# Performance work log

Measured on AMD Instinct MI355X. Metric: run time of the kernel, lower is better.

Reference implementation:

```python
import jax, jax.numpy as jnp
import numpy as np

# config: nsql-350M-like, 8 layers
L, D, H, HD, FF, V, RD, MP = 8, 1024, 16, 64, 4096, 51200, 32, 4


def setup_inputs() -> dict:
    key = jax.random.key(0)
    ks = jax.random.split(key, 8)
    B, S = 1, 1024
    s = 0.02
    return {
        'idx': jax.random.randint(ks[0], (B, S), 0, V),
        'input_pos': jnp.arange(S),
        'emb': jax.random.normal(ks[1], (V, D)) * s,
        'Wqkv': jax.random.normal(ks[2], (L, 3 * D, D)) * s,
        'Wo': jax.random.normal(ks[3], (L, D, D)) * s,
        'ln1_w': jnp.ones((L, D)), 'ln1_b': jnp.zeros((L, D)),
        'fc_in_w': jax.random.normal(ks[4], (L, FF, D)) * s,
        'fc_in_b': jnp.zeros((L, FF)),
        'fc_out_w': jax.random.normal(ks[5], (L, D, FF)) * s,
        'fc_out_b': jnp.zeros((L, D)),
        'lnf_w': jnp.ones((D,)), 'lnf_b': jnp.zeros((D,)),
        'lm_w': jax.random.normal(ks[6], (V, D)) * s,
        'lm_b': jnp.zeros((V,)),
    }


def _layer_norm(x, w, b, eps=1e-5):
    mu = jnp.mean(x, axis=-1, keepdims=True)
    var = jnp.var(x, axis=-1, keepdims=True)
    return (x - mu) * jax.lax.rsqrt(var + eps) * w + b


def _new_gelu(x):
    # transformers NewGELUActivation == tanh-approx gelu
    return jax.nn.gelu(x, approximate=True)


def _sincos(input_pos):
    # create_sinusoidal_positions over rotary_dim, gathered at input_pos
    inv_freq = 1.0 / (10000.0 ** (jnp.arange(0, RD, 2, dtype=jnp.float32) / RD))
    ang = input_pos.astype(jnp.float32)[:, None] * inv_freq          # [S, RD/2]
    # repeat_interleave(..., 2, dim=-1) -> interleaved sin/cos, shape [1,S,1,RD]
    sin = jnp.repeat(jnp.sin(ang), 2, axis=-1)[None, :, None, :]
    cos = jnp.repeat(jnp.cos(ang), 2, axis=-1)[None, :, None, :]
    return sin, cos


def _rotary(x, sin, cos):
    # x: [B,S,H,HD]; GPT-J interleaved rotary on first RD dims
    xr, xp = x[..., :RD], x[..., RD:]
    x1, x2 = xr[..., ::2], xr[..., 1::2]
    rot = jnp.stack((-x2, x1), axis=-1).reshape(xr.shape)  # rotate_every_two
    return jnp.concatenate([xr * cos + rot * sin, xp], axis=-1)


def reference(idx, input_pos, emb, Wqkv, Wo, ln1_w, ln1_b, fc_in_w, fc_in_b,
              fc_out_w, fc_out_b, lnf_w, lnf_b, lm_w, lm_b):
    B, S = idx.shape
    x = emb[idx]                                        # [B,S,D]
    sin, cos = _sincos(input_pos)
    causal = jnp.tril(jnp.ones((S, S), dtype=bool))
    neg = jnp.finfo(x.dtype).min
    ld = D // MP

    def split_heads(t):
        # CodeGen _split_heads with mp_num=4: [B,S,MP,ld] -> [B,S,H,HD]
        return t.reshape(B, S, MP, H // MP, HD).reshape(B, S, H, HD)

    for l in range(L):
        h = _layer_norm(x, ln1_w[l], ln1_b[l])
        qkv = (h @ Wqkv[l].T).reshape(B, S, MP, 3 * ld)
        q, v, k = qkv[..., :ld], qkv[..., ld:2 * ld], qkv[..., 2 * ld:]  # q,v,k order!
        q = _rotary(split_heads(q), sin, cos)
        k = _rotary(split_heads(k), sin, cos)
        vh = split_heads(v)
        q, k, vh = (jnp.transpose(t, (0, 2, 1, 3)) for t in (q, k, vh))  # [B,H,S,HD]
        scores = jnp.einsum('bhqd,bhkd->bhqk', q, k) / jnp.sqrt(jnp.asarray(HD, x.dtype))
        scores = jnp.where(causal, scores, neg)
        att = jax.nn.softmax(scores, axis=-1)
        y = jnp.einsum('bhqk,bhkd->bhqd', att, vh)
        y = jnp.transpose(y, (0, 2, 1, 3)).reshape(B, S, D)
        attn_out = y @ Wo[l].T
        mlp = _new_gelu(h @ fc_in_w[l].T + fc_in_b[l]) @ fc_out_w[l].T + fc_out_b[l]
        x = attn_out + mlp + x                          # parallel block + residual

    x = _layer_norm(x, lnf_w, lnf_b)
    return x @ lm_w.T + lm_b                            # [B,S,V]
```

## Files before the change

### kernel.cpp

```cpp
#include <hip/hip_runtime.h>

#define SQ 1024
#define DIM 1024
#define NH 16
#define HDIM 64
#define FFD 4096
#define NV 51200
#define NL 8
#define LDBUF 5120
#define WELEMS ((long)(3 * DIM + DIM + FFD + FFD) * DIM)

typedef __bf16 bf16x8 __attribute__((ext_vector_type(8)));
typedef float f32x4 __attribute__((ext_vector_type(4)));

__device__ __forceinline__ unsigned short f2bf(float f) {
    union { float f; unsigned int i; } v; v.f = f;
    unsigned int r = v.i + 0x7fffu + ((v.i >> 16) & 1u);
    return (unsigned short)(r >> 16);
}
__device__ __forceinline__ float gelu_tanh(float x) {
    float x3 = x * x * x;
    return 0.5f * x * (1.0f + tanhf(0.79788456080286535588f * (x + 0.044715f * x3)));
}
__device__ __forceinline__ void cvt8(const float* __restrict__ s, unsigned short* __restrict__ d, long i) {
    float4 a = *reinterpret_cast<const float4*>(s + i);
    float4 b = *reinterpret_cast<const float4*>(s + i + 4);
    bf16x8 w;
    w[0] = (__bf16)a.x; w[1] = (__bf16)a.y; w[2] = (__bf16)a.z; w[3] = (__bf16)a.w;
    w[4] = (__bf16)b.x; w[5] = (__bf16)b.y; w[6] = (__bf16)b.z; w[7] = (__bf16)b.w;
    *reinterpret_cast<bf16x8*>(d + i) = w;
}

#define GLD16(gp, lp) __builtin_amdgcn_global_load_lds( \
    (__attribute__((address_space(1))) void*)(gp), \
    (__attribute__((address_space(3))) void*)(lp), 16, 0, 0)
#define VMCNT0 asm volatile("s_waitcnt vmcnt(0)" ::: "memory")

__global__ void cvt4_kernel(const float* __restrict__ w0, const float* __restrict__ w1,
                            const float* __restrict__ w2, const float* __restrict__ w3,
                            unsigned short* __restrict__ dst) {
    const int b = blockIdx.x;
    const float* s; long off; unsigned short* d;
    if (b < 1536)      { s = w0; d = dst;                      off = (long)b * 2048; }
    else if (b < 2048) { s = w1; d = dst + (long)3072 * 1024;  off = (long)(b - 1536) * 2048; }
    else if (b < 4096) { s = w2; d = dst + (long)4096 * 1024;  off = (long)(b - 2048) * 2048; }
    else               { s = w3; d = dst + (long)8192 * 1024;  off = (long)(b - 4096) * 2048; }
    cvt8(s, d, off + threadIdx.x * 8);
}
__global__ void cvt_kernel(const float* __restrict__ src, unsigned short* __restrict__ dst) {
    cvt8(src, dst, ((long)blockIdx.x * 256 + threadIdx.x) * 8);
}

__global__ void sincos_kernel(const int* __restrict__ pos, float2* __restrict__ sc) {
    const int t = blockIdx.x * 256 + threadIdx.x;
    if (t >= SQ * 16) return;
    const int s = t >> 4, i = t & 15;
    const float ang = (float)pos[s] * powf(10000.0f, -(float)i / 16.0f);
    sc[t] = make_float2(sinf(ang), cosf(ang));
}

__global__ void embed_kernel(const int* __restrict__ idx, const float* __restrict__ emb,
                             float* __restrict__ x) {
    const int s = blockIdx.x;
    const int d = threadIdx.x * 4;
    const int row = idx[s];
    *reinterpret_cast<float4*>(x + (long)s * DIM + d) =
        *reinterpret_cast<const float4*>(emb + (long)row * DIM + d);
}

template <bool RED>
__global__ __launch_bounds__(256) void ln_kernel(float* __restrict__ x,
                                                 const float* __restrict__ part,
                                                 const float* __restrict__ w,
                                                 const float* __restrict__ b,
                                                 unsigned short* __restrict__ out) {
    __shared__ float red[8];
    const int s = blockIdx.x, tid = threadIdx.x;
    const long fidx = (long)s * 256 + tid;
    float4 v = reinterpret_cast<const float4*>(x)[fidx];
    if (RED) {
        #pragma unroll
        for (int z = 0; z < 4; z++) {
            float4 p = reinterpret_cast<const float4*>(part + (long)z * SQ * DIM)[fidx];
            v.x += p.x; v.y += p.y; v.z += p.z; v.w += p.w;
        }
        reinterpret_cast<float4*>(x)[fidx] = v;
    }
    float sum = v.x + v.y + v.z + v.w;
    float sq = v.x * v.x + v.y * v.y + v.z * v.z + v.w * v.w;
    #pragma unroll
    for (int off = 32; off; off >>= 1) { sum += __shfl_xor(sum, off); sq += __shfl_xor(sq, off); }
    const int wid = tid >> 6, lane = tid & 63;
    if (lane == 0) { red[wid * 2] = sum; red[wid * 2 + 1] = sq; }
    __syncthreads();
    sum = red[0] + red[2] + red[4] + red[6];
    sq  = red[1] + red[3] + red[5] + red[7];
    const float mu = sum * (1.0f / DIM);
    const float var = sq * (1.0f / DIM) - mu * mu;
    const float rstd = rsqrtf(var + 1e-5f);
    const int d = tid * 4;
    float vv[4] = {v.x, v.y, v.z, v.w};
    ushort4 o;
    unsigned short* op = (unsigned short*)&o;
    #pragma unroll
    for (int j = 0; j < 4; j++)
        op[j] = f2bf((vv[j] - mu) * rstd * w[d + j] + b[d + j]);
    *reinterpret_cast<ushort4*>(out + (long)s * DIM + d) = o;
}

__global__ __launch_bounds__(256) void gemm_qkv_fcin(const unsigned short* __restrict__ A,
                                                     const unsigned short* __restrict__ B1,
                                                     const unsigned short* __restrict__ B2,
                                                     const float* __restrict__ bias,
                                                     unsigned short* __restrict__ ffout,
                                                     const float2* __restrict__ sc,
                                                     unsigned short* __restrict__ qt,
                                                     unsigned short* __restrict__ kt,
                                                     unsigned short* __restrict__ vt,
                                                     const float* __restrict__ lmsrc,
                                                     unsigned short* __restrict__ lmdst) {
    __shared__ __align__(16) unsigned short As[2][128 * 64];
    __shared__ __align__(16) unsigned short Bs[2][128 * 64];
    const int tid = threadIdx.x;
    if (blockIdx.x >= 448) {
        if (lmdst) {
            const int cb = (int)blockIdx.x - 448;
            const long stride = (long)((int)gridDim.x - 448) * 256;
            const long nlmv = (long)(NV / NL) * DIM / 8;
            for (long i = (long)cb * 256 + tid; i < nlmv; i += stride) cvt8(lmsrc, lmdst, i * 8);
        }
        return;
    }
    const int sb = (blockIdx.x & 7) * 56 + (blockIdx.x >> 3);
    const int mb = sb & 7, nb = sb >> 3;
    const int m0 = mb * 128, n0 = nb * 128;
    const int lane = tid & 63, wid = tid >> 6;
    const int l15 = lane & 15, lhi = lane >> 4;
    const int wr = wid >> 1, wc = wid & 1;
    const int sw = l15 & 7;

    const unsigned short* Bbase = B1;
    int nloc = n0;
    if (nb >= 24) { Bbase = B2; nloc = n0 - 3072; }

    f32x4 acc[4][4];
    #pragma unroll
    for (int i = 0; i < 4; i++)
        #pragma unroll
        for (int j = 0; j < 4; j++) acc[i][j] = (f32x4){0.f, 0.f, 0.f, 0.f};

    const int wbase = (tid & ~63) * 8;

    auto stage = [&](int buf, int kt_) {
        const int k0 = kt_ << 6;
        #pragma unroll
        for (int i = 0; i < 4; i++) {
            const int e = (i * 256 + tid) * 8;
            const int r = e >> 6;
            const int cs = (((e >> 3) & 7) ^ (r & 7)) * 8;
            GLD16(A + (long)(m0 + r) * DIM + k0 + cs, &As[buf][i * 2048 + wbase]);
        }
        #pragma unroll
        for (int i = 0; i < 4; i++) {
            const int e = (i * 256 + tid) * 8;
            const int r = e >> 6;
            const int cs = (((e >> 3) & 7) ^ (r & 7)) * 8;
            GLD16(Bbase + (long)(nloc + r) * 1024 + k0 + cs, &Bs[buf][i * 2048 + wbase]);
        }
    };
    auto compute = [&](int buf) {
        #pragma unroll
        for (int ks = 0; ks < 2; ks++) {
            bf16x8 af[4], bfr[4];
            #pragma unroll
            for (int mf = 0; mf < 4; mf++)
                af[mf] = *reinterpret_cast<const bf16x8*>(
                    &As[buf][(wr * 64 + mf * 16 + l15) * 64 + ((ks * 4 + lhi) ^ sw) * 8]);
            #pragma unroll
            for (int nf = 0; nf < 4; nf++)
                bfr[nf] = *reinterpret_cast<const bf16x8*>(
                    &Bs[buf][(wc * 64 + nf * 16 + l15) * 64 + ((ks * 4 + lhi) ^ sw) * 8]);
            #pragma unroll
            for (int mf = 0; mf < 4; mf++)
                #pragma unroll
                for (int nf = 0; nf < 4; nf++)
                    acc[mf][nf] = __builtin_amdgcn_mfma_f32_16x16x32_bf16(af[mf], bfr[nf], acc[mf][nf], 0, 0, 0);
        }
    };

    int cur = 0;
    stage(0, 0);
    VMCNT0; __syncthreads();
    for (int kt_ = 0; kt_ < 16; kt_++) {
        if (kt_ + 1 < 16) stage(cur ^ 1, kt_ + 1);
        compute(cur);
        if (kt_ + 1 < 16) { VMCNT0; __syncthreads(); cur ^= 1; }
    }

    if (nb < 24) {
        #pragma unroll
        for (int nf = 0; nf < 4; nf++) {
            const int col = n0 + wc * 64 + nf * 16 + l15;
            const int g = col / 768;
            const int r768 = col - g * 768;
            const int sec = r768 >> 8;
            const int off = r768 & 255;
            const int h = g * 4 + (off >> 6);
            const int d = off & 63;
            const bool isrot = (d < 32);
            const int dodd = d & 1;
            #pragma unroll
            for (int mf = 0; mf < 4; mf++) {
                #pragma unroll
                for (int j = 0; j < 4; j++) {
                    const int row = m0 + wr * 64 + mf * 16 + lhi * 4 + j;
                    float v = acc[mf][nf][j];
                    const float pv = __shfl_xor(v, 1);
                    float outv = v;
                    if (isrot && sec != 1) {
                        const float2 scv = sc[row * 16 + (d >> 1)];
                        outv = dodd ? (v * scv.y + pv * scv.x)
                                    : (v * scv.y - pv * scv.x);
                    }
                    if (sec == 0)      qt[((long)(h * SQ + row)) * HDIM + d] = f2bf(outv);
                    else if (sec == 2) kt[((long)(h * SQ + row)) * HDIM + d] = f2bf(outv);
                    else               vt[(long)h * (HDIM * SQ) + (long)d * SQ + row] = f2bf(outv);
                }
            }
        }
    } else {
        #pragma unroll
        for (int nf = 0; nf < 4; nf++) {
            const int col = n0 + wc * 64 + nf * 16 + l15;
            #pragma unroll
            for (int mf = 0; mf < 4; mf++) {
                #pragma unroll
                for (int j = 0; j < 4; j++) {
                    const int row = m0 + wr * 64 + mf * 16 + lhi * 4 + j;
                    float v = gelu_tanh(acc[mf][nf][j] + bias[col - 3072]);
                    ffout[(long)row * LDBUF + (col - 3072)] = f2bf(v);
                }
            }
        }
    }
}

__global__ __launch_bounds__(256) void attn_fcout(const unsigned short* __restrict__ qt,
                                                  const unsigned short* __restrict__ kt,
                                                  const unsigned short* __restrict__ vt,
                                                  unsigned short* __restrict__ buf,
                                                  const unsigned short* __restrict__ fcw,
                                                  const float* __restrict__ fcb,
                                                  float* __restrict__ parts,
                                                  const float* __restrict__ nw0,
                                                  const float* __restrict__ nw1,
                                                  const float* __restrict__ nw2,
                                                  const float* __restrict__ nw3,
                                                  unsigned short* __restrict__ nd) {
    __shared__ __align__(16) unsigned short smem[32768];
    const int tid = threadIdx.x, lane = tid & 63, wid = tid >> 6;
    const int l15 = lane & 15, lhi = lane >> 4;
    const int sw = l15 & 7;
    const int wbase = (tid & ~63) * 8;

    if (blockIdx.x < 256) {
        unsigned short* Ks0 = smem;
        unsigned short* Vs0 = smem + 8192;
        unsigned short* Psw = smem + 16384 + wid * 1024;
        const int h = blockIdx.x & 15;
        const int qb = 15 - ((int)blockIdx.x >> 4);
        const int q0 = qb * 64 + wid * 16;

        bf16x8 aq[2];
        {
            const unsigned short* qp = qt + ((long)(h * SQ + q0 + l15)) * HDIM;
            aq[0] = *reinterpret_cast<const bf16x8*>(qp + lhi * 8);
            aq[1] = *reinterpret_cast<const bf16x8*>(qp + 32 + lhi * 8);
        }
        f32x4 o[4];
        #pragma unroll
        for (int nf = 0; nf < 4; nf++) o[nf] = (f32x4){0.f, 0.f, 0.f, 0.f};
        float mrow[4] = {-1e30f, -1e30f, -1e30f, -1e30f};
        float lrow[4] = {0.f, 0.f, 0.f, 0.f};

        auto stageKV = [&](int b, int kv0) {
            #pragma unroll
            for (int i = 0; i < 2; i++) {
                const int e = (i * 256 + tid) * 8;
                const int r = e >> 6;
                const int cs = (((e >> 3) & 7) ^ (r & 7)) * 8;
                GLD16(kt + ((long)(h * SQ + kv0 + r)) * HDIM + cs, Ks0 + b * 4096 + i * 2048 + wbase);
                GLD16(vt + (long)h * (HDIM * SQ) + (long)r * SQ + kv0 + cs, Vs0 + b * 4096 + i * 2048 + wbase);
            }
        };

        int cur = 0;
        stageKV(0, 0);
        VMCNT0; __syncthreads();
        for (int kvt = 0; kvt <= qb; kvt++) {
            const int kv0 = kvt * 64;
            if (kvt < qb) stageKV(cur ^ 1, kv0 + 64);

            f32x4 sa[4];
            #pragma unroll
            for (int hc = 0; hc < 4; hc++) sa[hc] = (f32x4){0.f, 0.f, 0.f, 0.f};
            #pragma unroll
            for (int hc = 0; hc < 4; hc++)
                #pragma unroll
                for (int ks = 0; ks < 2; ks++) {
                    bf16x8 bk = *reinterpret_cast<const bf16x8*>(
                        Ks0 + cur * 4096 + (hc * 16 + l15) * 64 + ((ks * 4 + lhi) ^ sw) * 8);
                    sa[hc] = __builtin_amdgcn_mfma_f32_16x16x32_bf16(aq[ks], bk, sa[hc], 0, 0, 0);
                }
            float pr[4][4], mb[4];
            #pragma unroll
            for (int j = 0; j < 4; j++) {
                const int qi = q0 + lhi * 4 + j;
                #pragma unroll
                for (int hc = 0; hc < 4; hc++) {
                    const int ki = kv0 + hc * 16 + l15;
                    const float sv = sa[hc][j] * 0.125f;
                    pr[hc][j] = (ki <= qi) ? sv : -1e30f;
                }
                mb[j] = fmaxf(fmaxf(pr[0][j], pr[1][j]), fmaxf(pr[2][j], pr[3][j]));
            }
            #pragma unroll
            for (int off = 1; off < 16; off <<= 1)
                #pragma unroll
                for (int j = 0; j < 4; j++) mb[j] = fmaxf(mb[j], __shfl_xor(mb[j], off));
            float alpha[4], psum[4];
            #pragma unroll
            for (int j = 0; j < 4; j++) {
                const float mn = fmaxf(mrow[j], mb[j]);
                alpha[j] = __expf(mrow[j] - mn);
                mrow[j] = mn;
                psum[j] = 0.f;
                #pragma unroll
                for (int hc = 0; hc < 4; hc++) { pr[hc][j] = __expf(pr[hc][j] - mn); psum[j] += pr[hc][j]; }
            }
            #pragma unroll
            for (int off = 1; off < 16; off <<= 1)
                #pragma unroll
                for (int j = 0; j < 4; j++) psum[j] += __shfl_xor(psum[j], off);
            #pragma unroll
            for (int j = 0; j < 4; j++) lrow[j] = lrow[j] * alpha[j] + psum[j];
            #pragma unroll
            for (int nf = 0; nf < 4; nf++)
                #pragma unroll
                for (int j = 0; j < 4; j++) o[nf][j] *= alpha[j];
            #pragma unroll
            for (int hc = 0; hc < 4; hc++)
                #pragma unroll
                for (int j = 0; j < 4; j++) {
                    const int prow = lhi * 4 + j;
                    const int pc8 = (hc * 2 + (l15 >> 3)) ^ (prow & 7);
                    Psw[prow * 64 + pc8 * 8 + (l15 & 7)] = f2bf(pr[hc][j]);
                }
            bf16x8 ap[2];
            ap[0] = *reinterpret_cast<const bf16x8*>(Psw + l15 * 64 + ((0 + lhi) ^ sw) * 8);
            ap[1] = *reinterpret_cast<const bf16x8*>(Psw + l15 * 64 + ((4 + lhi) ^ sw) * 8);
            #pragma unroll
            for (int nf = 0; nf < 4; nf++)
                #pragma unroll
                for (int ks2 = 0; ks2 < 2; ks2++) {
                    bf16x8 bv = *reinterpret_cast<const bf16x8*>(
                        Vs0 + cur * 4096 + (nf * 16 + l15) * 64 + ((ks2 * 4 + lhi) ^ sw) * 8);
                    o[nf] = __builtin_amdgcn_mfma_f32_16x16x32_bf16(ap[ks2], bv, o[nf], 0, 0, 0);
                }
            if (kvt < qb) { VMCNT0; __syncthreads(); cur ^= 1; }
        }
        #pragma unroll
        for (int nf = 0; nf < 4; nf++)
            #pragma unroll
            for (int j = 0; j < 4; j++) {
                const int row = q0 + lhi * 4 + j;
                buf[(long)row * LDBUF + h * HDIM + nf * 16 + l15] = f2bf(o[nf][j] / lrow[j]);
            }
    } else if (blockIdx.x < 512) {
        unsigned short* As0 = smem;
        unsigned short* Bs0 = smem + 16384;
        const int b2 = (int)blockIdx.x - 256;
        const int sb = (b2 & 7) * 32 + (b2 >> 3);
        const int kz = sb & 3, nb = (sb >> 2) & 7, mb = sb >> 5;
        const int m0 = mb * 128, n0 = nb * 128;
        const int kt0 = kz * 16;
        const int wr = wid >> 1, wc = wid & 1;
        const unsigned short* Aff = buf + DIM;

        f32x4 acc[4][4];
        #pragma unroll
        for (int i = 0; i < 4; i++)
            #pragma unroll
            for (int j = 0; j < 4; j++) acc[i][j] = (f32x4){0.f, 0.f, 0.f, 0.f};

        auto stage = [&](int bf_, int kt_) {
            const int k0 = kt_ << 6;
            #pragma unroll
            for (int i = 0; i < 4; i++) {
                const int e = (i * 256 + tid) * 8;
                const int r = e >> 6;
                const int cs = (((e >> 3) & 7) ^ (r & 7)) * 8;
                GLD16(Aff + (long)(m0 + r) * LDBUF + k0 + cs, As0 + bf_ * 8192 + i * 2048 + wbase);
                GLD16(fcw + (long)(n0 + r) * FFD + k0 + cs, Bs0 + bf_ * 8192 + i * 2048 + wbase);
            }
        };
        auto compute = [&](int bf_) {
            #pragma unroll
            for (int ks = 0; ks < 2; ks++) {
                bf16x8 af[4], bfr[4];
                #pragma unroll
                for (int mf = 0; mf < 4; mf++)
                    af[mf] = *reinterpret_cast<const bf16x8*>(
                        As0 + bf_ * 8192 + (wr * 64 + mf * 16 + l15) * 64 + ((ks * 4 + lhi) ^ sw) * 8);
                #pragma unroll
                for (int nf = 0; nf < 4; nf++)
                    bfr[nf] = *reinterpret_cast<const bf16x8*>(
                        Bs0 + bf_ * 8192 + (wc * 64 + nf * 16 + l15) * 64 + ((ks * 4 + lhi) ^ sw) * 8);
                #pragma unroll
                for (int mf = 0; mf < 4; mf++)
                    #pragma unroll
                    for (int nf = 0; nf < 4; nf++)
                        acc[mf][nf] = __builtin_amdgcn_mfma_f32_16x16x32_bf16(af[mf], bfr[nf], acc[mf][nf], 0, 0, 0);
            }
        };

        int cur = 0;
        stage(0, kt0);
        VMCNT0; __syncthreads();
        for (int t = 0; t < 16; t++) {
            if (t + 1 < 16) stage(cur ^ 1, kt0 + t + 1);
            compute(cur);
            if (t + 1 < 16) { VMCNT0; __syncthreads(); cur ^= 1; }
        }

        float* P = parts + (long)kz * SQ * DIM;
        #pragma unroll
        for (int nf = 0; nf < 4; nf++) {
            const int col = n0 + wc * 64 + nf * 16 + l15;
            const float bv = (kz == 0) ? fcb[col] : 0.f;
            #pragma unroll
            for (int mf = 0; mf < 4; mf++) {
                #pragma unroll
                for (int j = 0; j < 4; j++) {
                    const int row = m0 + wr * 64 + mf * 16 + lhi * 4 + j;
                    P[(long)row * DIM + col] = acc[mf][nf][j] + bv;
                }
            }
        }
    } else {
        if (nd) {
            const int cb = (int)blockIdx.x - 512;
            const long stride = (long)((int)gridDim.x - 512) * 256;
            const long base = (long)cb * 256 + tid;
            const long n0v = (long)3072 * 1024 / 8, n1v = (long)1024 * 1024 / 8;
            const long n2v = (long)4096 * 1024 / 8, n3v = (long)4096 * 1024 / 8;
            for (long i = base; i < n0v; i += stride) cvt8(nw0, nd, i * 8);
            unsigned short* d1 = nd + n0v * 8;
            for (long i = base; i < n1v; i += stride) cvt8(nw1, d1, i * 8);
            unsigned short* d2 = d1 + n1v * 8;
            for (long i = base; i < n2v; i += stride) cvt8(nw2, d2, i * 8);
            unsigned short* d3 = d2 + n2v * 8;
            for (long i = base; i < n3v; i += stride) cvt8(nw3, d3, i * 8);
        }
    }
}

__global__ __launch_bounds__(256) void wo_rmw(const unsigned short* __restrict__ buf,
                                              const unsigned short* __restrict__ wo,
                                              float* __restrict__ parts) {
    __shared__ __align__(16) unsigned short As[2][128 * 64];
    __shared__ __align__(16) unsigned short Bs[2][128 * 64];
    const int tid = threadIdx.x;
    const int sb = (blockIdx.x & 7) * 32 + (blockIdx.x >> 3);
    const int kz = sb & 3, nb = (sb >> 2) & 7, mb = sb >> 5;
    const int m0 = mb * 128, n0 = nb * 128;
    const int kt0 = kz * 4;
    const int lane = tid & 63, wid = tid >> 6;
    const int l15 = lane & 15, lhi = lane >> 4;
    const int wr = wid >> 1, wc = wid & 1;
    const int sw = l15 & 7;
    const int wbase = (tid & ~63) * 8;

    f32x4 acc[4][4];
    #pragma unroll
    for (int i = 0; i < 4; i++)
        #pragma unroll
        for (int j = 0; j < 4; j++) acc[i][j] = (f32x4){0.f, 0.f, 0.f, 0.f};

    auto stage = [&](int bf_, int kt_) {
        const int k0 = kt_ << 6;
        #pragma unroll
        for (int i = 0; i < 4; i++) {
            const int e = (i * 256 + tid) * 8;
            const int r = e >> 6;
            const int cs = (((e >> 3) & 7) ^ (r & 7)) * 8;
            GLD16(buf + (long)(m0 + r) * LDBUF + k0 + cs, &As[bf_][i * 2048 + wbase]);
            GLD16(wo + (long)(n0 + r) * DIM + k0 + cs, &Bs[bf_][i * 2048 + wbase]);
        }
    };
    auto compute = [&](int bf_) {
        #pragma unroll
        for (int ks = 0; ks < 2; ks++) {
            bf16x8 af[4], bfr[4];
            #pragma unroll
            for (int mf = 0; mf < 4; mf++)
                af[mf] = *reinterpret_cast<const bf16x8*>(
                    &As[bf_][(wr * 64 + mf * 16 + l15) * 64 + ((ks * 4 + lhi) ^ sw) * 8]);
            #pragma unroll
            for (int nf = 0; nf < 4; nf++)
                bfr[nf] = *reinterpret_cast<const bf16x8*>(
                    &Bs[bf_][(wc * 64 + nf * 16 + l15) * 64 + ((ks * 4 + lhi) ^ sw) * 8]);
            #pragma unroll
            for (int mf = 0; mf < 4; mf++)
                #pragma unroll
                for (int nf = 0; nf < 4; nf++)
                    acc[mf][nf] = __builtin_amdgcn_mfma_f32_16x16x32_bf16(af[mf], bfr[nf], acc[mf][nf], 0, 0, 0);
        }
    };

    int cur = 0;
    stage(0, kt0);
    VMCNT0; __syncthreads();
    for (int t = 0; t < 4; t++) {
        if (t + 1 < 4) stage(cur ^ 1, kt0 + t + 1);
        compute(cur);
        if (t + 1 < 4) { VMCNT0; __syncthreads(); cur ^= 1; }
    }

    float* P = parts + (long)kz * SQ * DIM;
    #pragma unroll
    for (int nf = 0; nf < 4; nf++) {
        const int col = n0 + wc * 64 + nf * 16 + l15;
        #pragma unroll
        for (int mf = 0; mf < 4; mf++) {
            #pragma unroll
            for (int j = 0; j < 4; j++) {
                const int row = m0 + wr * 64 + mf * 16 + lhi * 4 + j;
                P[(long)row * DIM + col] += acc[mf][nf][j];
            }
        }
    }
}

__global__ __launch_bounds__(512) void gemm256(const unsigned short* __restrict__ A,
                                               const unsigned short* __restrict__ B,
                                               const float* __restrict__ bias,
                                               float* __restrict__ C) {
    __shared__ __align__(16) unsigned short As[2][256 * 64];
    __shared__ __align__(16) unsigned short Bs[2][256 * 64];
    const int tid = threadIdx.x;
    const int nwg = gridDim.x, qch = nwg >> 3;
    const int sb = (blockIdx.x & 7) * qch + (blockIdx.x >> 3);
    const int mb = sb & 3, nb = sb >> 2;
    const int m0 = mb * 256, n0 = nb * 256;
    const int lane = tid & 63, wid = tid >> 6;
    const int l15 = lane & 15, lhi = lane >> 4;
    const int wm = wid >> 2, wn = wid & 3;
    const int sw = l15 & 7;

    f32x4 acc[8][4];
    #pragma unroll
    for (int i = 0; i < 8; i++)
        #pragma unroll
        for (int j = 0; j < 4; j++) acc[i][j] = (f32x4){0.f, 0.f, 0.f, 0.f};

    const int wbase = (tid & ~63) * 8;

    auto stage = [&](int buf, int kt) {
        const int k0 = kt << 6;
        #pragma unroll
        for (int i = 0; i < 4; i++) {
            const int e = (i * 512 + tid) * 8;
            const int r = e >> 6;
            const int cs = (((e >> 3) & 7) ^ (r & 7)) * 8;
            GLD16(A + (long)(m0 + r) * 1024 + k0 + cs, &As[buf][i * 4096 + wbase]);
            GLD16(B + (long)(n0 + r) * 1024 + k0 + cs, &Bs[buf][i * 4096 + wbase]);
        }
    };
    auto compute = [&](int buf) {
        #pragma unroll
        for (int ks = 0; ks < 2; ks++) {
            bf16x8 af[8], bfr[4];
            #pragma unroll
            for (int mf = 0; mf < 8; mf++)
                af[mf] = *reinterpret_cast<const bf16x8*>(
                    &As[buf][(wm * 128 + mf * 16 + l15) * 64 + ((ks * 4 + lhi) ^ sw) * 8]);
            #pragma unroll
            for (int nf = 0; nf < 4; nf++)
                bfr[nf] = *reinterpret_cast<const bf16x8*>(
                    &Bs[buf][(wn * 64 + nf * 16 + l15) * 64 + ((ks * 4 + lhi) ^ sw) * 8]);
            #pragma unroll
            for (int mf = 0; mf < 8; mf++)
                #pragma unroll
                for (int nf = 0; nf < 4; nf++)
                    acc[mf][nf] = __builtin_amdgcn_mfma_f32_16x16x32_bf16(af[mf], bfr[nf], acc[mf][nf], 0, 0, 0);
        }
    };

    int cur = 0;
    stage(0, 0);
    VMCNT0; __syncthreads();
    for (int kt = 0; kt < 16; kt++) {
        if (kt < 15) stage(cur ^ 1, kt + 1);
        compute(cur);
        if (kt < 15) { VMCNT0; __syncthreads(); cur ^= 1; }
    }

    #pragma unroll
    for (int nf = 0; nf < 4; nf++) {
        const int col = n0 + wn * 64 + nf * 16 + l15;
        const float bv = bias[col];
        #pragma unroll
        for (int mf = 0; mf < 8; mf++) {
            #pragma unroll
            for (int j = 0; j < 4; j++) {
                const int row = m0 + wm * 128 + mf * 16 + lhi * 4 + j;
                C[(long)row * NV + col] = acc[mf][nf][j] + bv;
            }
        }
    }
}

__global__ __launch_bounds__(256) void gemm128lm(const unsigned short* __restrict__ A,
                                                 const unsigned short* __restrict__ B,
                                                 const float* __restrict__ bias,
                                                 float* __restrict__ C, int coff) {
    __shared__ __align__(16) unsigned short As[2][128 * 64];
    __shared__ __align__(16) unsigned short Bs[2][128 * 64];
    const int tid = threadIdx.x;
    const int nwg = gridDim.x, qch = nwg >> 3;
    const int sb = (blockIdx.x & 7) * qch + (blockIdx.x >> 3);
    const int mb = sb & 7, nb = sb >> 3;
    const int m0 = mb * 128, n0 = coff + nb * 128;
    const int lane = tid & 63, wid = tid >> 6;
    const int l15 = lane & 15, lhi = lane >> 4;
    const int wr = wid >> 1, wc = wid & 1;
    const int sw = l15 & 7;
    const int wbase = (tid & ~63) * 8;

    f32x4 acc[4][4];
    #pragma unroll
    for (int i = 0; i < 4; i++)
        #pragma unroll
        for (int j = 0; j < 4; j++) acc[i][j] = (f32x4){0.f, 0.f, 0.f, 0.f};

    auto stage = [&](int buf, int kt_) {
        const int k0 = kt_ << 6;
        #pragma unroll
        for (int i = 0; i < 4; i++) {
            const int e = (i * 256 + tid) * 8;
            const int r = e >> 6;
            const int cs = (((e >> 3) & 7) ^ (r & 7)) * 8;
            GLD16(A + (long)(m0 + r) * 1024 + k0 + cs, &As[buf][i * 2048 + wbase]);
            GLD16(B + (long)(n0 + r) * 1024 + k0 + cs, &Bs[buf][i * 2048 + wbase]);
        }
    };
    auto compute = [&](int buf) {
        #pragma unroll
        for (int ks = 0; ks < 2; ks++) {
            bf16x8 af[4], bfr[4];
            #pragma unroll
            for (int mf = 0; mf < 4; mf++)
                af[mf] = *reinterpret_cast<const bf16x8*>(
                    &As[buf][(wr * 64 + mf * 16 + l15) * 64 + ((ks * 4 + lhi) ^ sw) * 8]);
            #pragma unroll
            for (int nf = 0; nf < 4; nf++)
                bfr[nf] = *reinterpret_cast<const bf16x8*>(
                    &Bs[buf][(wc * 64 + nf * 16 + l15) * 64 + ((ks * 4 + lhi) ^ sw) * 8]);
            #pragma unroll
            for (int mf = 0; mf < 4; mf++)
                #pragma unroll
                for (int nf = 0; nf < 4; nf++)
                    acc[mf][nf] = __builtin_amdgcn_mfma_f32_16x16x32_bf16(af[mf], bfr[nf], acc[mf][nf], 0, 0, 0);
        }
    };

    int cur = 0;
    stage(0, 0);
    VMCNT0; __syncthreads();
    for (int kt_ = 0; kt_ < 16; kt_++) {
        if (kt_ + 1 < 16) stage(cur ^ 1, kt_ + 1);
        compute(cur);
        if (kt_ + 1 < 16) { VMCNT0; __syncthreads(); cur ^= 1; }
    }

    #pragma unroll
    for (int nf = 0; nf < 4; nf++) {
        const int col = n0 + wc * 64 + nf * 16 + l15;
        const float bv = bias[col];
        #pragma unroll
        for (int mf = 0; mf < 4; mf++) {
            #pragma unroll
            for (int j = 0; j < 4; j++) {
                const int row = m0 + wr * 64 + mf * 16 + lhi * 4 + j;
                C[(long)row * NV + col] = acc[mf][nf][j] + bv;
            }
        }
    }
}

extern "C" void kernel_launch(void* const* d_in, const int* in_sizes, int n_in,
                              void* d_out, int out_size, void* d_ws, size_t ws_size,
                              hipStream_t stream) {
    const int* idx    = (const int*)d_in[0];
    const int* pos    = (const int*)d_in[1];
    const float* emb  = (const float*)d_in[2];
    const float* Wqkv = (const float*)d_in[3];
    const float* Wo   = (const float*)d_in[4];
    const float* ln1w = (const float*)d_in[5];
    const float* ln1b = (const float*)d_in[6];
    const float* fciw = (const float*)d_in[7];
    const float* fcib = (const float*)d_in[8];
    const float* fcow = (const float*)d_in[9];
    const float* fcob = (const float*)d_in[10];
    const float* lnfw = (const float*)d_in[11];
    const float* lnfb = (const float*)d_in[12];
    const float* lmw  = (const float*)d_in[13];
    const float* lmb  = (const float*)d_in[14];

    const long tailBytes = (long)SQ * DIM * 4 + (long)4 * SQ * DIM * 4 + (long)SQ * DIM * 2
                         + (long)3 * NH * SQ * HDIM * 2 + (long)SQ * LDBUF * 2 + (long)SQ * 16 * 8;
    const long bigBytes  = 2 * WELEMS * 2 + (long)NV * DIM * 2 + tailBytes;
    const bool big = (long)ws_size >= bigBytes + (1 << 20);

    char* ws = (char*)d_ws;
    unsigned short *wbufA, *wbufB, *lmbuf;
    if (big) {
        wbufA = (unsigned short*)ws; ws += WELEMS * 2;
        wbufB = (unsigned short*)ws; ws += WELEMS * 2;
        lmbuf = (unsigned short*)ws; ws += (long)NV * DIM * 2;
    } else {
        wbufA = (unsigned short*)ws; ws += (long)NV * DIM * 2;
        wbufB = wbufA;
        lmbuf = wbufA;
    }
    float* x           = (float*)ws;          ws += (long)SQ * DIM * 4;
    float* parts       = (float*)ws;          ws += (long)4 * SQ * DIM * 4;
    unsigned short* h  = (unsigned short*)ws; ws += (long)SQ * DIM * 2;
    unsigned short* qt = (unsigned short*)ws; ws += (long)NH * SQ * HDIM * 2;
    unsigned short* kt = (unsigned short*)ws; ws += (long)NH * SQ * HDIM * 2;
    unsigned short* vt = (unsigned short*)ws; ws += (long)NH * SQ * HDIM * 2;
    unsigned short* buf= (unsigned short*)ws; ws += (long)SQ * LDBUF * 2;
    float2* sc         = (float2*)ws;         ws += (long)SQ * 16 * 8;

    auto wq = [&](unsigned short* wb) { return wb; };
    auto wo_ = [&](unsigned short* wb) { return wb + (long)3072 * 1024; };
    auto wfi = [&](unsigned short* wb) { return wb + (long)4096 * 1024; };
    auto wfo = [&](unsigned short* wb) { return wb + (long)8192 * 1024; };

    sincos_kernel<<<64, 256, 0, stream>>>(pos, sc);
    embed_kernel<<<SQ, 256, 0, stream>>>(idx, emb, x);
    cvt4_kernel<<<6144, 256, 0, stream>>>(Wqkv, Wo, fciw, fcow, wbufA);

    for (int l = 0; l < NL; l++) {
        unsigned short* wb = (l & 1) ? wbufB : wbufA;
        unsigned short* wn = (l & 1) ? wbufA : wbufB;

        if (!big && l > 0)
            cvt4_kernel<<<6144, 256, 0, stream>>>(Wqkv + (long)l * 3 * DIM * DIM,
                                                  Wo   + (long)l * DIM * DIM,
                                                  fciw + (long)l * FFD * DIM,
                                                  fcow + (long)l * DIM * FFD, wb);

        if (l == 0) ln_kernel<false><<<SQ, 256, 0, stream>>>(x, nullptr, ln1w, ln1b, h);
        else ln_kernel<true><<<SQ, 256, 0, stream>>>(x, parts, ln1w + (long)l * DIM, ln1b + (long)l * DIM, h);

        gemm_qkv_fcin<<<704, 256, 0, stream>>>(h, wq(wb), wfi(wb), fcib + (long)l * FFD,
                                               buf + DIM, sc, qt, kt, vt,
                                               big ? lmw + (long)l * (NV / NL) * DIM : nullptr,
                                               big ? lmbuf + (long)l * (NV / NL) * DIM : nullptr);
        if (big) {
            const int nl = l + 1;
            attn_fcout<<<1024, 256, 0, stream>>>(qt, kt, vt, buf, wfo(wb),
                                                 fcob + (long)l * DIM, parts,
                                                 (nl < NL) ? Wqkv + (long)nl * 3 * DIM * DIM : nullptr,
                                                 (nl < NL) ? Wo   + (long)nl * DIM * DIM : nullptr,
                                                 (nl < NL) ? fciw + (long)nl * FFD * DIM : nullptr,
                                                 (nl < NL) ? fcow + (long)nl * DIM * FFD : nullptr,
                                                 (nl < NL) ? wn : nullptr);
        } else {
            attn_fcout<<<512, 256, 0, stream>>>(qt, kt, vt, buf, wfo(wb),
                                                fcob + (long)l * DIM, parts,
                                                nullptr, nullptr, nullptr, nullptr, nullptr);
        }
        wo_rmw<<<256, 256, 0, stream>>>(buf, wo_(wb), parts);
    }
    if (!big) cvt_kernel<<<25600, 256, 0, stream>>>(lmw, lmbuf);
    ln_kernel<true><<<SQ, 256, 0, stream>>>(x, parts, lnfw, lnfb, h);
    gemm256<<<400, 512, 0, stream>>>(h, lmbuf, lmb, (float*)d_out);
    gemm128lm<<<1600, 256, 0, stream>>>(h, lmbuf, lmb, (float*)d_out, 25600);
}
```

Measured before the change: 1.053 ms.

## Add 8-phase ping-pong 256x256 LM-head GEMM and rebalance column split

Adds a 256x256-tile LM-head GEMM whose A and B stages are split into 128-row halves. Global loads for later k-tiles are interleaved with four MFMA quarter-blocks per k-tile, using fine-grained barriers, partial vmcnt waits and s_setprio. The column split also changes: the new kernel covers the first 38400 vocab columns and the original double-buffered 256 kernel (now taking a column offset) covers the rest, replacing the 128-tile kernel. This aims to hide load latency behind MFMA work in the largest GEMM, at the cost of many more barriers and more complex scheduling.

```diff
diff --git a/kernel.cpp b/kernel.cpp
--- a/kernel.cpp
+++ b/kernel.cpp
@@ -542,12 +542,12 @@
     }
 }
 
-__global__ __launch_bounds__(512) void gemm256(const unsigned short* __restrict__ A,
-                                               const unsigned short* __restrict__ B,
-                                               const float* __restrict__ bias,
-                                               float* __restrict__ C) {
-    __shared__ __align__(16) unsigned short As[2][256 * 64];
-    __shared__ __align__(16) unsigned short Bs[2][256 * 64];
+__global__ __launch_bounds__(512) void gemm256p8(const unsigned short* __restrict__ A,
+                                                 const unsigned short* __restrict__ B,
+                                                 const float* __restrict__ bias,
+                                                 float* __restrict__ C) {
+    __shared__ __align__(16) unsigned short As[2][2][128 * 64];
+    __shared__ __align__(16) unsigned short Bs[2][2][128 * 64];
     const int tid = threadIdx.x;
     const int nwg = gridDim.x, qch = nwg >> 3;
     const int sb = (blockIdx.x & 7) * qch + (blockIdx.x >> 3);
@@ -557,6 +557,140 @@
     const int l15 = lane & 15, lhi = lane >> 4;
     const int wm = wid >> 2, wn = wid & 3;
     const int sw = l15 & 7;
+    const int wbase = (tid & ~63) * 8;
+
+    f32x4 acc[8][4];
+    #pragma unroll
+    for (int i = 0; i < 8; i++)
+        #pragma unroll
+        for (int j = 0; j < 4; j++) acc[i][j] = (f32x4){0.f, 0.f, 0.f, 0.f};
+
+    auto stageA = [&](int kt, int hh) {
+        const int k0 = kt << 6;
+        unsigned short* dst = &As[kt & 1][hh][0];
+        #pragma unroll
+        for (int i = 0; i < 2; i++) {
+            const int e = (i * 512 + tid) * 8;
+            const int r = e >> 6;
+            const int cs = (((e >> 3) & 7) ^ (r & 7)) * 8;
+            GLD16(A + (long)(m0 + hh * 128 + r) * 1024 + k0 + cs, dst + i * 4096 + wbase);
+        }
+    };
+    auto stageB = [&](int kt, int hh) {
+        const int k0 = kt << 6;
+        unsigned short* dst = &Bs[kt & 1][hh][0];
+        #pragma unroll
+        for (int i = 0; i < 2; i++) {
+            const int e = (i * 512 + tid) * 8;
+            const int r = e >> 6;
+            const int cs = (((e >> 3) & 7) ^ (r & 7)) * 8;
+            GLD16(B + (long)(n0 + hh * 128 + r) * 1024 + k0 + cs, dst + i * 4096 + wbase);
+        }
+    };
+
+    bf16x8 afA[4][2], bf0[2][2], bf1[2][2];
+    auto ldA = [&](int buf, int hh) {
+        #pragma unroll
+        for (int mi = 0; mi < 4; mi++) {
+            const int row = wm * 64 + mi * 16 + l15;
+            #pragma unroll
+            for (int ks = 0; ks < 2; ks++)
+                afA[mi][ks] = *reinterpret_cast<const bf16x8*>(
+                    &As[buf][hh][row * 64 + (((ks * 4 + lhi) ^ sw) * 8)]);
+        }
+    };
+    auto ldB = [&](int buf, int hh, bf16x8 (&bfr)[2][2]) {
+        #pragma unroll
+        for (int ni = 0; ni < 2; ni++) {
+            const int row = wn * 32 + ni * 16 + l15;
+            #pragma unroll
+            for (int ks = 0; ks < 2; ks++)
+                bfr[ni][ks] = *reinterpret_cast<const bf16x8*>(
+                    &Bs[buf][hh][row * 64 + (((ks * 4 + lhi) ^ sw) * 8)]);
+        }
+    };
+    auto mfma16 = [&](int mh, int nh, bf16x8 (&bfr)[2][2]) {
+        __builtin_amdgcn_s_setprio(1);
+        #pragma unroll
+        for (int mi = 0; mi < 4; mi++)
+            #pragma unroll
+            for (int ni = 0; ni < 2; ni++)
+                #pragma unroll
+                for (int ks = 0; ks < 2; ks++)
+                    acc[mh * 4 + mi][nh * 2 + ni] = __builtin_amdgcn_mfma_f32_16x16x32_bf16(
+                        afA[mi][ks], bfr[ni][ks], acc[mh * 4 + mi][nh * 2 + ni], 0, 0, 0);
+        __builtin_amdgcn_s_setprio(0);
+    };
+
+#define BAR()   __builtin_amdgcn_s_barrier()
+#define LGKM()  asm volatile("s_waitcnt lgkmcnt(0)" ::: "memory")
+#define VM6()   asm volatile("s_waitcnt vmcnt(6)" ::: "memory")
+
+    stageA(0, 0); stageB(0, 0); stageB(0, 1); stageA(0, 1);
+    stageA(1, 0); stageB(1, 0); stageB(1, 1);
+    VM6();
+    BAR();
+
+    for (int it = 0; it < 8; it++) {
+        const int e = 2 * it, o = 2 * it + 1;
+        const bool more = (it + 1 < 8);
+        ldA(0, 0); ldB(0, 0, bf0);
+        stageA(o, 1);
+        BAR(); LGKM(); mfma16(0, 0, bf0); BAR();
+        ldB(0, 1, bf1);
+        if (more) stageA(e + 2, 0);
+        BAR(); LGKM(); mfma16(0, 1, bf1); BAR();
+        ldA(0, 1);
+        if (more) stageB(e + 2, 0);
+        BAR(); LGKM(); mfma16(1, 1, bf1); BAR();
+        if (more) stageB(e + 2, 1);
+        if (more) { VM6(); } else { VMCNT0; }
+        BAR(); LGKM(); mfma16(1, 0, bf0); BAR();
+        ldA(1, 0); ldB(1, 0, bf0);
+        if (more) stageA(e + 2, 1);
+        BAR(); LGKM(); mfma16(0, 0, bf0); BAR();
+        ldB(1, 1, bf1);
+        if (more) stageA(o + 2, 0);
+        BAR(); LGKM(); mfma16(0, 1, bf1); BAR();
+        ldA(1, 1);
+        if (more) stageB(o + 2, 0);
+        BAR(); LGKM(); mfma16(1, 1, bf1); BAR();
+        if (more) { stageB(o + 2, 1); VM6(); }
+        BAR(); LGKM(); mfma16(1, 0, bf0); BAR();
+    }
+#undef BAR
+#undef LGKM
+#undef VM6
+
+    #pragma unroll
+    for (int nf = 0; nf < 4; nf++) {
+        const int col = n0 + (nf < 2 ? wn * 32 + nf * 16 : 128 + wn * 32 + (nf - 2) * 16) + l15;
+        const float bv = bias[col];
+        #pragma unroll
+        for (int mf = 0; mf < 8; mf++) {
+            const int rowb = m0 + (mf < 4 ? wm * 64 + mf * 16 : 128 + wm * 64 + (mf - 4) * 16) + lhi * 4;
+            #pragma unroll
+            for (int j = 0; j < 4; j++)
+                C[(long)(rowb + j) * NV + col] = acc[mf][nf][j] + bv;
+        }
+    }
+}
+
+__global__ __launch_bounds__(512) void gemm256(const unsigned short* __restrict__ A,
+                                               const unsigned short* __restrict__ B,
+                                               const float* __restrict__ bias,
+                                               float* __restrict__ C, int coff) {
+    __shared__ __align__(16) unsigned short As[2][256 * 64];
+    __shared__ __align__(16) unsigned short Bs[2][256 * 64];
+    const int tid = threadIdx.x;
+    const int nwg = gridDim.x, qch = nwg >> 3;
+    const int sb = (blockIdx.x & 7) * qch + (blockIdx.x >> 3);
+    const int mb = sb & 3, nb = sb >> 2;
+    const int m0 = mb * 256, n0 = coff + nb * 256;
+    const int lane = tid & 63, wid = tid >> 6;
+    const int l15 = lane & 15, lhi = lane >> 4;
+    const int wm = wid >> 2, wn = wid & 3;
+    const int sw = l15 & 7;
 
     f32x4 acc[8][4];
     #pragma unroll
@@ -615,84 +749,6 @@
             #pragma unroll
             for (int j = 0; j < 4; j++) {
                 const int row = m0 + wm * 128 + mf * 16 + lhi * 4 + j;
-                C[(long)row * NV + col] = acc[mf][nf][j] + bv;
-            }
-        }
-    }
-}
-
-__global__ __launch_bounds__(256) void gemm128lm(const unsigned short* __restrict__ A,
-                                                 const unsigned short* __restrict__ B,
-                                                 const float* __restrict__ bias,
-                                                 float* __restrict__ C, int coff) {
-    __shared__ __align__(16) unsigned short As[2][128 * 64];
-    __shared__ __align__(16) unsigned short Bs[2][128 * 64];
-    const int tid = threadIdx.x;
-    const int nwg = gridDim.x, qch = nwg >> 3;
-    const int sb = (blockIdx.x & 7) * qch + (blockIdx.x >> 3);
-    const int mb = sb & 7, nb = sb >> 3;
-    const int m0 = mb * 128, n0 = coff + nb * 128;
-    const int lane = tid & 63, wid = tid >> 6;
-    const int l15 = lane & 15, lhi = lane >> 4;
-    const int wr = wid >> 1, wc = wid & 1;
-    const int sw = l15 & 7;
-    const int wbase = (tid & ~63) * 8;
-
-    f32x4 acc[4][4];
-    #pragma unroll
-    for (int i = 0; i < 4; i++)
-        #pragma unroll
-        for (int j = 0; j < 4; j++) acc[i][j] = (f32x4){0.f, 0.f, 0.f, 0.f};
-
-    auto stage = [&](int buf, int kt_) {
-        const int k0 = kt_ << 6;
-        #pragma unroll
-        for (int i = 0; i < 4; i++) {
-            const int e = (i * 256 + tid) * 8;
-            const int r = e >> 6;
-            const int cs = (((e >> 3) & 7) ^ (r & 7)) * 8;
-            GLD16(A + (long)(m0 + r) * 1024 + k0 + cs, &As[buf][i * 2048 + wbase]);
-            GLD16(B + (long)(n0 + r) * 1024 + k0 + cs, &Bs[buf][i * 2048 + wbase]);
-        }
-    };
-    auto compute = [&](int buf) {
-        #pragma unroll
-        for (int ks = 0; ks < 2; ks++) {
-            bf16x8 af[4], bfr[4];
-            #pragma unroll
-            for (int mf = 0; mf < 4; mf++)
-                af[mf] = *reinterpret_cast<const bf16x8*>(
-                    &As[buf][(wr * 64 + mf * 16 + l15) * 64 + ((ks * 4 + lhi) ^ sw) * 8]);
-            #pragma unroll
-            for (int nf = 0; nf < 4; nf++)
-                bfr[nf] = *reinterpret_cast<const bf16x8*>(
-                    &Bs[buf][(wc * 64 + nf * 16 + l15) * 64 + ((ks * 4 + lhi) ^ sw) * 8]);
-            #pragma unroll
-            for (int mf = 0; mf < 4; mf++)
-                #pragma unroll
-                for (int nf = 0; nf < 4; nf++)
-                    acc[mf][nf] = __builtin_amdgcn_mfma_f32_16x16x32_bf16(af[mf], bfr[nf], acc[mf][nf], 0, 0, 0);
-        }
-    };
-
-    int cur = 0;
-    stage(0, 0);
-    VMCNT0; __syncthreads();
-    for (int kt_ = 0; kt_ < 16; kt_++) {
-        if (kt_ + 1 < 16) stage(cur ^ 1, kt_ + 1);
-        compute(cur);
-        if (kt_ + 1 < 16) { VMCNT0; __syncthreads(); cur ^= 1; }
-    }
-
-    #pragma unroll
-    for (int nf = 0; nf < 4; nf++) {
-        const int col = n0 + wc * 64 + nf * 16 + l15;
-        const float bv = bias[col];
-        #pragma unroll
-        for (int mf = 0; mf < 4; mf++) {
-            #pragma unroll
-            for (int j = 0; j < 4; j++) {
-                const int row = m0 + wr * 64 + mf * 16 + lhi * 4 + j;
                 C[(long)row * NV + col] = acc[mf][nf][j] + bv;
             }
         }
@@ -787,6 +843,6 @@
     }
     if (!big) cvt_kernel<<<25600, 256, 0, stream>>>(lmw, lmbuf);
     ln_kernel<true><<<SQ, 256, 0, stream>>>(x, parts, lnfw, lnfb, h);
-    gemm256<<<400, 512, 0, stream>>>(h, lmbuf, lmb, (float*)d_out);
-    gemm128lm<<<1600, 256, 0, stream>>>(h, lmbuf, lmb, (float*)d_out, 25600);
-}
+    gemm256p8<<<600, 512, 0, stream>>>(h, lmbuf, lmb, (float*)d_out);
+    gemm256<<<200, 512, 0, stream>>>(h, lmbuf, lmb, (float*)d_out, 38400);
+}
```

Result: faster. 983.7 us (-6.6%).
